# Performance work log

Measured on AMD Instinct MI355X. Metric: run time of the kernel, lower is better.

The kernel has to match this reference:

```python
import jax, jax.numpy as jnp
import numpy as np

B, N, D = 256, 50, 128
NEG = -9e15  # torch uses -9000000000000000.0
LEAKY_SLOPE = 0.2


def setup_inputs() -> dict:
    key = jax.random.key(0)
    ks = jax.random.split(key, 6)
    hidden = jax.random.normal(ks[0], (B, N, D), dtype=jnp.float32)
    adj = jax.random.randint(ks[1], (B, N, N), 0, 5)  # edge types 0..4
    a_0 = jax.random.normal(ks[2], (D, 1), dtype=jnp.float32) * 0.05
    a_1 = jax.random.normal(ks[3], (D, 1), dtype=jnp.float32) * 0.05
    a_2 = jax.random.normal(ks[4], (D, 1), dtype=jnp.float32) * 0.05
    a_3 = jax.random.normal(ks[5], (D, 1), dtype=jnp.float32) * 0.05
    return {"hidden": hidden, "adj": adj, "a_0": a_0, "a_1": a_1, "a_2": a_2, "a_3": a_3}


def reference(hidden, adj, a_0, a_1, a_2, a_3):
    # LocalAggregator.forward (typed-edge GAT over session graph).
    # Original builds a_input[b,i,j,:] = h[b,i,:]*h[b,j,:] (B,N,N,D) then
    # projects with 4 relation vectors a_k (D,1). We fuse: stack the 4
    # vectors and contract D in one einsum -> e[b,k,i,j].
    A = jnp.concatenate([a_0, a_1, a_2, a_3], axis=1)          # (D, 4)
    e = jnp.einsum('bid,bjd,dk->bkij', hidden, hidden, A)      # (B, 4, N, N)
    e = jax.nn.leaky_relu(e, negative_slope=LEAKY_SLOPE)
    # Per-edge-type masking: adj value v in {1..4} selects branch v-1,
    # anything else gets -9e15 (same chained torch.where semantics/order).
    scores = jnp.full_like(e[:, 0], NEG)                        # (B, N, N)
    scores = jnp.where(adj == 1, e[:, 0], scores)
    scores = jnp.where(adj == 2, e[:, 1], scores)
    scores = jnp.where(adj == 3, e[:, 2], scores)
    scores = jnp.where(adj == 4, e[:, 3], scores)
    attn = jax.nn.softmax(scores, axis=-1)                      # (B, N, N)
    return jnp.einsum('bij,bjd->bid', attn, hidden)             # (B, N, D)
```

## Files before the change

### kernel.cpp

```cpp
#include <hip/hip_runtime.h>
#include <stdint.h>

typedef __attribute__((ext_vector_type(8))) short short8;
typedef __attribute__((ext_vector_type(4))) float f32x4;

namespace {
constexpr int   kN     = 50;
constexpr int   kD     = 128;
constexpr float kNeg   = -9.0e15f;
constexpr float kSlope = 0.2f;
constexpr int   HS32   = 132;
constexpr int   HS16   = 136;
constexpr int   SS     = 68;
constexpr int   AS     = 52;
}

union Pack8 { uint32_t u[4]; short8 s; };

__global__ __launch_bounds__(512)
void gat_mfma_kernel(const float* __restrict__ hidden,
                     const int*   __restrict__ adj,
                     const float* __restrict__ a0,
                     const float* __restrict__ a1,
                     const float* __restrict__ a2,
                     const float* __restrict__ a3,
                     float* __restrict__ out)
{
    __shared__ float          Hf [kN * HS32];
    __shared__ unsigned short Hhi[kN * HS16];
    __shared__ unsigned short Hlo[kN * HS16];
    __shared__ float          Af [4 * HS32];
    __shared__ float          Sa [kN * SS];
    __shared__ float          Sb [kN * SS];
    __shared__ float          At [64 * AS];

    const int b    = blockIdx.x;
    const int tid  = threadIdx.x;
    const int lane = tid & 63;
    const int wid  = tid >> 6;

    const float* __restrict__ hb   = hidden + (size_t)b * (kN * kD);
    const int*   __restrict__ adjb = adj    + (size_t)b * (kN * kN);
    float*       __restrict__ outb = out    + (size_t)b * (kN * kD);

    const float4* hg = reinterpret_cast<const float4*>(hb);
    for (int idx = tid; idx < kN * (kD / 4); idx += 512) {
        const int j  = idx >> 5;
        const int d4 = idx & 31;
        const float4 v = hg[idx];
        *reinterpret_cast<float4*>(&Hf[j * HS32 + 4 * d4]) = v;

        const uint32_t u0 = __float_as_uint(v.x), u1 = __float_as_uint(v.y);
        const uint32_t u2 = __float_as_uint(v.z), u3 = __float_as_uint(v.w);
        const uint32_t h0 = u0 & 0xffff0000u, h1 = u1 & 0xffff0000u;
        const uint32_t h2 = u2 & 0xffff0000u, h3 = u3 & 0xffff0000u;
        uint2 hiw;
        hiw.x = h1 | (h0 >> 16);
        hiw.y = h3 | (h2 >> 16);
        const float r0 = v.x - __uint_as_float(h0);
        const float r1 = v.y - __uint_as_float(h1);
        const float r2 = v.z - __uint_as_float(h2);
        const float r3 = v.w - __uint_as_float(h3);
        uint2 low;
        low.x = (__float_as_uint(r1) & 0xffff0000u) | (__float_as_uint(r0) >> 16);
        low.y = (__float_as_uint(r3) & 0xffff0000u) | (__float_as_uint(r2) >> 16);
        *reinterpret_cast<uint2*>(&Hhi[j * HS16 + 4 * d4]) = hiw;
        *reinterpret_cast<uint2*>(&Hlo[j * HS16 + 4 * d4]) = low;
    }
    if (tid < 128) {
        const int k  = tid >> 5;
        const int d4 = tid & 31;
        const float* ap = (k == 0) ? a0 : (k == 1) ? a1 : (k == 2) ? a2 : a3;
        *reinterpret_cast<float4*>(&Af[k * HS32 + 4 * d4]) =
            *reinterpret_cast<const float4*>(ap + 4 * d4);
    }
    __syncthreads();

    {
        const int it = wid & 3;
        const int kh = wid >> 2;
        const int i0 = it * 16;
        const int g  = lane >> 4;
        const int f  = lane & 15;
        const int irow = (i0 + f < kN) ? (i0 + f) : (kN - 1);

        f32x4 acc[4][4];
        #pragma unroll
        for (int jt = 0; jt < 4; ++jt)
            #pragma unroll
            for (int k = 0; k < 4; ++k)
                acc[jt][k] = (f32x4){0.f, 0.f, 0.f, 0.f};

        #pragma unroll
        for (int ksl = 0; ksl < 2; ++ksl) {
            const int ks   = 2 * kh + ksl;
            const int dofs = 32 * ks + 8 * g;

            const float4 hA0 = *reinterpret_cast<const float4*>(&Hf[irow * HS32 + dofs]);
            const float4 hA1 = *reinterpret_cast<const float4*>(&Hf[irow * HS32 + dofs + 4]);
            float ha[8] = {hA0.x, hA0.y, hA0.z, hA0.w, hA1.x, hA1.y, hA1.z, hA1.w};

            short8 qhi[4], qlo[4];
            #pragma unroll
            for (int k = 0; k < 4; ++k) {
                const float4 av0 = *reinterpret_cast<const float4*>(&Af[k * HS32 + dofs]);
                const float4 av1 = *reinterpret_cast<const float4*>(&Af[k * HS32 + dofs + 4]);
                const float aa[8] = {av0.x, av0.y, av0.z, av0.w, av1.x, av1.y, av1.z, av1.w};
                Pack8 ph, pl;
                #pragma unroll
                for (int p = 0; p < 4; ++p) {
                    const float q0 = ha[2 * p]     * aa[2 * p];
                    const float q1 = ha[2 * p + 1] * aa[2 * p + 1];
                    const uint32_t b0 = __float_as_uint(q0) & 0xffff0000u;
                    const uint32_t b1 = __float_as_uint(q1) & 0xffff0000u;
                    ph.u[p] = b1 | (b0 >> 16);
                    const float s0 = q0 - __uint_as_float(b0);
                    const float s1 = q1 - __uint_as_float(b1);
                    pl.u[p] = (__float_as_uint(s1) & 0xffff0000u) | (__float_as_uint(s0) >> 16);
                }
                qhi[k] = ph.s;
                qlo[k] = pl.s;
            }

            #pragma unroll
            for (int jt = 0; jt < 4; ++jt) {
                const int jrow = (jt * 16 + f < kN) ? (jt * 16 + f) : (kN - 1);
                const short8 bh = *reinterpret_cast<const short8*>(&Hhi[jrow * HS16 + dofs]);
                const short8 bl = *reinterpret_cast<const short8*>(&Hlo[jrow * HS16 + dofs]);
                #pragma unroll
                for (int k = 0; k < 4; ++k) {
                    acc[jt][k] = __builtin_amdgcn_mfma_f32_16x16x32_bf16(qhi[k], bh, acc[jt][k], 0, 0, 0);
                    acc[jt][k] = __builtin_amdgcn_mfma_f32_16x16x32_bf16(qhi[k], bl, acc[jt][k], 0, 0, 0);
                    acc[jt][k] = __builtin_amdgcn_mfma_f32_16x16x32_bf16(qlo[k], bh, acc[jt][k], 0, 0, 0);
                }
            }
        }

        float* Sbuf = (kh == 0) ? Sa : Sb;
        #pragma unroll
        for (int jt = 0; jt < 4; ++jt) {
            const int j = jt * 16 + f;
            #pragma unroll
            for (int reg = 0; reg < 4; ++reg) {
                const int ii = i0 + 4 * g + reg;
                int adjv = 0;
                if (ii < kN && j < kN) adjv = adjb[ii * kN + j];
                const float val = (adjv == 1) ? acc[jt][0][reg]
                                : (adjv == 2) ? acc[jt][1][reg]
                                : (adjv == 3) ? acc[jt][2][reg]
                                : (adjv == 4) ? acc[jt][3][reg] : 0.f;
                if (ii < kN) Sbuf[ii * SS + j] = val;
            }
        }
    }
    __syncthreads();

    for (int r = wid; r < kN; r += 8) {
        const float x = Sa[r * SS + lane] + Sb[r * SS + lane];
        int adjv = 0;
        if (lane < kN) adjv = adjb[r * kN + lane];
        const bool valid = (adjv >= 1) && (adjv <= 4);
        const float lx = (x > 0.f) ? x : kSlope * x;
        float s = valid ? lx : kNeg;
        float m = s;
        #pragma unroll
        for (int o = 32; o; o >>= 1) m = fmaxf(m, __shfl_xor(m, o));
        const float e = (lane < kN) ? __expf(s - m) : 0.f;
        float t = e;
        #pragma unroll
        for (int o = 32; o; o >>= 1) t += __shfl_xor(t, o);
        At[lane * AS + r] = e / t;
    }
    __syncthreads();

    {
        const int it = wid & 3;
        const int dh = wid >> 2;
        const int i0 = it * 16;
        const int g  = lane >> 4;
        const int f  = lane & 15;
        const int db = 64 * dh + 4 * f;

        float4 o0 = {0.f, 0.f, 0.f, 0.f}, o1 = o0, o2 = o0, o3 = o0;
        #pragma unroll 5
        for (int j = 0; j < kN; ++j) {
            const float4 hv = *reinterpret_cast<const float4*>(&Hf[j * HS32 + db]);
            const float4 av = *reinterpret_cast<const float4*>(&At[j * AS + i0 + 4 * g]);
            o0.x += av.x * hv.x; o0.y += av.x * hv.y; o0.z += av.x * hv.z; o0.w += av.x * hv.w;
            o1.x += av.y * hv.x; o1.y += av.y * hv.y; o1.z += av.y * hv.z; o1.w += av.y * hv.w;
            o2.x += av.z * hv.x; o2.y += av.z * hv.y; o2.z += av.z * hv.z; o2.w += av.z * hv.w;
            o3.x += av.w * hv.x; o3.y += av.w * hv.y; o3.z += av.w * hv.z; o3.w += av.w * hv.w;
        }
        const int rbase = i0 + 4 * g;
        if (rbase + 0 < kN) *reinterpret_cast<float4*>(&outb[(rbase + 0) * kD + db]) = o0;
        if (rbase + 1 < kN) *reinterpret_cast<float4*>(&outb[(rbase + 1) * kD + db]) = o1;
        if (rbase + 2 < kN) *reinterpret_cast<float4*>(&outb[(rbase + 2) * kD + db]) = o2;
        if (rbase + 3 < kN) *reinterpret_cast<float4*>(&outb[(rbase + 3) * kD + db]) = o3;
    }
}

extern "C" void kernel_launch(void* const* d_in, const int* in_sizes, int n_in,
                              void* d_out, int out_size, void* d_ws, size_t ws_size,
                              hipStream_t stream) {
    const float* hidden = reinterpret_cast<const float*>(d_in[0]);
    const int*   adjp   = reinterpret_cast<const int*>(d_in[1]);
    const float* a0     = reinterpret_cast<const float*>(d_in[2]);
    const float* a1     = reinterpret_cast<const float*>(d_in[3]);
    const float* a2     = reinterpret_cast<const float*>(d_in[4]);
    const float* a3     = reinterpret_cast<const float*>(d_in[5]);
    float*       outp   = reinterpret_cast<float*>(d_out);

    gat_mfma_kernel<<<dim3(256), dim3(512), 0, stream>>>(
        hidden, adjp, a0, a1, a2, a3, outp);
}
```

Baseline: 20.06 us.

## Split each batch across two blocks by row halves and store attention as bf16

Launches two blocks per batch element, each handling half of the query rows, so 512 blocks run instead of 256. Each wave now owns one j-tile over the full D range, which removes the split-K partial score buffers and their reduction. The a_k vectors are read straight from global memory instead of staged in shared memory. Attention weights are stored as bf16 to cut LDS footprint. The trade-off is that hidden is loaded and split twice per batch, half the waves idle in the final aggregation, and bf16 attention weights lose precision.

```diff
diff --git a/kernel.cpp b/kernel.cpp
--- a/kernel.cpp
+++ b/kernel.cpp
@@ -12,48 +12,51 @@
 constexpr int   HS32   = 132;
 constexpr int   HS16   = 136;
 constexpr int   SS     = 68;
-constexpr int   AS     = 52;
+constexpr int   AS     = 36;
 }
 
 union Pack8 { uint32_t u[4]; short8 s; };
 
 __global__ __launch_bounds__(512)
-void gat_mfma_kernel(const float* __restrict__ hidden,
-                     const int*   __restrict__ adj,
-                     const float* __restrict__ a0,
-                     const float* __restrict__ a1,
-                     const float* __restrict__ a2,
-                     const float* __restrict__ a3,
-                     float* __restrict__ out)
+void gat_v6_kernel(const float* __restrict__ hidden,
+                   const int*   __restrict__ adj,
+                   const float* __restrict__ a0,
+                   const float* __restrict__ a1,
+                   const float* __restrict__ a2,
+                   const float* __restrict__ a3,
+                   float* __restrict__ out)
 {
     __shared__ float          Hf [kN * HS32];
-    __shared__ unsigned short Hhi[kN * HS16];
-    __shared__ unsigned short Hlo[kN * HS16];
-    __shared__ float          Af [4 * HS32];
-    __shared__ float          Sa [kN * SS];
-    __shared__ float          Sb [kN * SS];
-    __shared__ float          At [64 * AS];
-
-    const int b    = blockIdx.x;
+    __shared__ unsigned short Hhi[64 * HS16];
+    __shared__ unsigned short Hlo[64 * HS16];
+    __shared__ float          Sa [32 * SS];
+    __shared__ unsigned short At [64 * AS];
+
+    const int b    = blockIdx.x >> 1;
+    const int ih   = blockIdx.x & 1;
     const int tid  = threadIdx.x;
     const int lane = tid & 63;
-    const int wid  = tid >> 6;
+    const int wid  = __builtin_amdgcn_readfirstlane(tid >> 6);
+    const int g    = lane >> 4;
+    const int f    = lane & 15;
 
     const float* __restrict__ hb   = hidden + (size_t)b * (kN * kD);
     const int*   __restrict__ adjb = adj    + (size_t)b * (kN * kN);
     float*       __restrict__ outb = out    + (size_t)b * (kN * kD);
 
     const float4* hg = reinterpret_cast<const float4*>(hb);
-    for (int idx = tid; idx < kN * (kD / 4); idx += 512) {
-        const int j  = idx >> 5;
-        const int d4 = idx & 31;
-        const float4 v = hg[idx];
-        *reinterpret_cast<float4*>(&Hf[j * HS32 + 4 * d4]) = v;
-
-        const uint32_t u0 = __float_as_uint(v.x), u1 = __float_as_uint(v.y);
-        const uint32_t u2 = __float_as_uint(v.z), u3 = __float_as_uint(v.w);
-        const uint32_t h0 = u0 & 0xffff0000u, h1 = u1 & 0xffff0000u;
-        const uint32_t h2 = u2 & 0xffff0000u, h3 = u3 & 0xffff0000u;
+    #pragma unroll
+    for (int it4 = 0; it4 < 4; ++it4) {
+        const int idx = tid + it4 * 512;
+        const int j   = idx >> 5;
+        const int d4  = idx & 31;
+        float4 v = make_float4(0.f, 0.f, 0.f, 0.f);
+        if (j < kN) v = hg[j * 32 + d4];
+
+        const uint32_t h0 = __float_as_uint(v.x) & 0xffff0000u;
+        const uint32_t h1 = __float_as_uint(v.y) & 0xffff0000u;
+        const uint32_t h2 = __float_as_uint(v.z) & 0xffff0000u;
+        const uint32_t h3 = __float_as_uint(v.w) & 0xffff0000u;
         uint2 hiw;
         hiw.x = h1 | (h0 >> 16);
         hiw.y = h3 | (h2 >> 16);
@@ -66,45 +69,45 @@
         low.y = (__float_as_uint(r3) & 0xffff0000u) | (__float_as_uint(r2) >> 16);
         *reinterpret_cast<uint2*>(&Hhi[j * HS16 + 4 * d4]) = hiw;
         *reinterpret_cast<uint2*>(&Hlo[j * HS16 + 4 * d4]) = low;
-    }
-    if (tid < 128) {
-        const int k  = tid >> 5;
-        const int d4 = tid & 31;
-        const float* ap = (k == 0) ? a0 : (k == 1) ? a1 : (k == 2) ? a2 : a3;
-        *reinterpret_cast<float4*>(&Af[k * HS32 + 4 * d4]) =
-            *reinterpret_cast<const float4*>(ap + 4 * d4);
+        if (j < kN) *reinterpret_cast<float4*>(&Hf[j * HS32 + 4 * d4]) = v;
     }
     __syncthreads();
 
     {
-        const int it = wid & 3;
-        const int kh = wid >> 2;
-        const int i0 = it * 16;
-        const int g  = lane >> 4;
-        const int f  = lane & 15;
+        const int jt   = wid & 3;
+        const int itL  = wid >> 2;
+        const int itG  = 2 * ih + itL;
+        const int i0   = 16 * itG;
         const int irow = (i0 + f < kN) ? (i0 + f) : (kN - 1);
-
-        f32x4 acc[4][4];
-        #pragma unroll
-        for (int jt = 0; jt < 4; ++jt)
-            #pragma unroll
-            for (int k = 0; k < 4; ++k)
-                acc[jt][k] = (f32x4){0.f, 0.f, 0.f, 0.f};
-
-        #pragma unroll
-        for (int ksl = 0; ksl < 2; ++ksl) {
-            const int ks   = 2 * kh + ksl;
-            const int dofs = 32 * ks + 8 * g;
-
-            const float4 hA0 = *reinterpret_cast<const float4*>(&Hf[irow * HS32 + dofs]);
-            const float4 hA1 = *reinterpret_cast<const float4*>(&Hf[irow * HS32 + dofs + 4]);
-            float ha[8] = {hA0.x, hA0.y, hA0.z, hA0.w, hA1.x, hA1.y, hA1.z, hA1.w};
-
-            short8 qhi[4], qlo[4];
+        const int jrow = 16 * jt + f;
+
+        f32x4 acc[4];
+        #pragma unroll
+        for (int k = 0; k < 4; ++k) acc[k] = (f32x4){0.f, 0.f, 0.f, 0.f};
+
+        const float* __restrict__ aks[4] = {a0, a1, a2, a3};
+
+        #pragma unroll
+        for (int ksl = 0; ksl < 4; ++ksl) {
+            const int dofs = 32 * ksl + 8 * g;
+
+            const short8 ah8 = *reinterpret_cast<const short8*>(&Hhi[irow * HS16 + dofs]);
+            const short8 al8 = *reinterpret_cast<const short8*>(&Hlo[irow * HS16 + dofs]);
+            float ha[8];
+            #pragma unroll
+            for (int p = 0; p < 8; ++p) {
+                const uint32_t uh = ((uint32_t)(unsigned short)ah8[p]) << 16;
+                const uint32_t ul = ((uint32_t)(unsigned short)al8[p]) << 16;
+                ha[p] = __uint_as_float(uh) + __uint_as_float(ul);
+            }
+
+            const short8 bh = *reinterpret_cast<const short8*>(&Hhi[jrow * HS16 + dofs]);
+            const short8 bl = *reinterpret_cast<const short8*>(&Hlo[jrow * HS16 + dofs]);
+
             #pragma unroll
             for (int k = 0; k < 4; ++k) {
-                const float4 av0 = *reinterpret_cast<const float4*>(&Af[k * HS32 + dofs]);
-                const float4 av1 = *reinterpret_cast<const float4*>(&Af[k * HS32 + dofs + 4]);
+                const float4 av0 = *reinterpret_cast<const float4*>(aks[k] + dofs);
+                const float4 av1 = *reinterpret_cast<const float4*>(aks[k] + dofs + 4);
                 const float aa[8] = {av0.x, av0.y, av0.z, av0.w, av1.x, av1.y, av1.z, av1.w};
                 Pack8 ph, pl;
                 #pragma unroll
@@ -118,84 +121,89 @@
                     const float s1 = q1 - __uint_as_float(b1);
                     pl.u[p] = (__float_as_uint(s1) & 0xffff0000u) | (__float_as_uint(s0) >> 16);
                 }
-                qhi[k] = ph.s;
-                qlo[k] = pl.s;
-            }
-
-            #pragma unroll
-            for (int jt = 0; jt < 4; ++jt) {
-                const int jrow = (jt * 16 + f < kN) ? (jt * 16 + f) : (kN - 1);
-                const short8 bh = *reinterpret_cast<const short8*>(&Hhi[jrow * HS16 + dofs]);
-                const short8 bl = *reinterpret_cast<const short8*>(&Hlo[jrow * HS16 + dofs]);
-                #pragma unroll
-                for (int k = 0; k < 4; ++k) {
-                    acc[jt][k] = __builtin_amdgcn_mfma_f32_16x16x32_bf16(qhi[k], bh, acc[jt][k], 0, 0, 0);
-                    acc[jt][k] = __builtin_amdgcn_mfma_f32_16x16x32_bf16(qhi[k], bl, acc[jt][k], 0, 0, 0);
-                    acc[jt][k] = __builtin_amdgcn_mfma_f32_16x16x32_bf16(qlo[k], bh, acc[jt][k], 0, 0, 0);
-                }
-            }
-        }
-
-        float* Sbuf = (kh == 0) ? Sa : Sb;
-        #pragma unroll
-        for (int jt = 0; jt < 4; ++jt) {
-            const int j = jt * 16 + f;
-            #pragma unroll
-            for (int reg = 0; reg < 4; ++reg) {
-                const int ii = i0 + 4 * g + reg;
-                int adjv = 0;
-                if (ii < kN && j < kN) adjv = adjb[ii * kN + j];
-                const float val = (adjv == 1) ? acc[jt][0][reg]
-                                : (adjv == 2) ? acc[jt][1][reg]
-                                : (adjv == 3) ? acc[jt][2][reg]
-                                : (adjv == 4) ? acc[jt][3][reg] : 0.f;
-                if (ii < kN) Sbuf[ii * SS + j] = val;
+                acc[k] = __builtin_amdgcn_mfma_f32_16x16x32_bf16(ph.s, bh, acc[k], 0, 0, 0);
+                acc[k] = __builtin_amdgcn_mfma_f32_16x16x32_bf16(ph.s, bl, acc[k], 0, 0, 0);
+                acc[k] = __builtin_amdgcn_mfma_f32_16x16x32_bf16(pl.s, bh, acc[k], 0, 0, 0);
+            }
+        }
+
+        const int j = 16 * jt + f;
+        #pragma unroll
+        for (int reg = 0; reg < 4; ++reg) {
+            const int iL = 16 * itL + 4 * g + reg;
+            const int ii = 32 * ih + iL;
+            if (ii < kN && j < kN) {
+                const int adjv = adjb[ii * kN + j];
+                const float val = (adjv == 1) ? acc[0][reg]
+                                : (adjv == 2) ? acc[1][reg]
+                                : (adjv == 3) ? acc[2][reg]
+                                : (adjv == 4) ? acc[3][reg] : 0.f;
+                Sa[iL * SS + j] = val;
             }
         }
     }
     __syncthreads();
 
-    for (int r = wid; r < kN; r += 8) {
-        const float x = Sa[r * SS + lane] + Sb[r * SS + lane];
-        int adjv = 0;
-        if (lane < kN) adjv = adjb[r * kN + lane];
-        const bool valid = (adjv >= 1) && (adjv <= 4);
-        const float lx = (x > 0.f) ? x : kSlope * x;
-        float s = valid ? lx : kNeg;
-        float m = s;
-        #pragma unroll
-        for (int o = 32; o; o >>= 1) m = fmaxf(m, __shfl_xor(m, o));
-        const float e = (lane < kN) ? __expf(s - m) : 0.f;
-        float t = e;
-        #pragma unroll
-        for (int o = 32; o; o >>= 1) t += __shfl_xor(t, o);
-        At[lane * AS + r] = e / t;
+    {
+        const int icount = ih ? (kN - 32) : 32;
+        float attv[4];
+        #pragma unroll
+        for (int t = 0; t < 4; ++t) {
+            const int rL = wid + 8 * t;
+            const int r  = 32 * ih + rL;
+            const bool rowv = (rL < icount);
+            const float x = Sa[rL * SS + lane];
+            int adjv = 0;
+            if (rowv && lane < kN) adjv = adjb[r * kN + lane];
+            const bool valid = (adjv >= 1) && (adjv <= 4);
+            const float lx = (x > 0.f) ? x : kSlope * x;
+            float s = valid ? lx : kNeg;
+            float m = s;
+            #pragma unroll
+            for (int o = 32; o; o >>= 1) m = fmaxf(m, __shfl_xor(m, o));
+            const float e = (lane < kN) ? __expf(s - m) : 0.f;
+            float ts = e;
+            #pragma unroll
+            for (int o = 32; o; o >>= 1) ts += __shfl_xor(ts, o);
+            attv[t] = e / ts;
+        }
+        #pragma unroll
+        for (int t = 0; t < 4; ++t) {
+            const int rL = wid + 8 * t;
+            if (rL < icount) {
+                uint32_t u = __float_as_uint(attv[t]);
+                u += 0x7fffu + ((u >> 16) & 1u);
+                At[lane * AS + rL] = (unsigned short)(u >> 16);
+            }
+        }
     }
     __syncthreads();
 
-    {
-        const int it = wid & 3;
-        const int dh = wid >> 2;
-        const int i0 = it * 16;
-        const int g  = lane >> 4;
-        const int f  = lane & 15;
-        const int db = 64 * dh + 4 * f;
-
-        float4 o0 = {0.f, 0.f, 0.f, 0.f}, o1 = o0, o2 = o0, o3 = o0;
+    if (wid < 4) {
+        const int itL = wid & 1;
+        const int dh  = wid >> 1;
+        const int i0L = 16 * itL;
+        const int db  = 64 * dh + 4 * f;
+
+        f32x4 o0 = {0.f, 0.f, 0.f, 0.f}, o1 = o0, o2 = o0, o3 = o0;
         #pragma unroll 5
         for (int j = 0; j < kN; ++j) {
-            const float4 hv = *reinterpret_cast<const float4*>(&Hf[j * HS32 + db]);
-            const float4 av = *reinterpret_cast<const float4*>(&At[j * AS + i0 + 4 * g]);
-            o0.x += av.x * hv.x; o0.y += av.x * hv.y; o0.z += av.x * hv.z; o0.w += av.x * hv.w;
-            o1.x += av.y * hv.x; o1.y += av.y * hv.y; o1.z += av.y * hv.z; o1.w += av.y * hv.w;
-            o2.x += av.z * hv.x; o2.y += av.z * hv.y; o2.z += av.z * hv.z; o2.w += av.z * hv.w;
-            o3.x += av.w * hv.x; o3.y += av.w * hv.y; o3.z += av.w * hv.z; o3.w += av.w * hv.w;
-        }
-        const int rbase = i0 + 4 * g;
-        if (rbase + 0 < kN) *reinterpret_cast<float4*>(&outb[(rbase + 0) * kD + db]) = o0;
-        if (rbase + 1 < kN) *reinterpret_cast<float4*>(&outb[(rbase + 1) * kD + db]) = o1;
-        if (rbase + 2 < kN) *reinterpret_cast<float4*>(&outb[(rbase + 2) * kD + db]) = o2;
-        if (rbase + 3 < kN) *reinterpret_cast<float4*>(&outb[(rbase + 3) * kD + db]) = o3;
+            const float4  hv = *reinterpret_cast<const float4*>(&Hf[j * HS32 + db]);
+            const ushort4 a4 = *reinterpret_cast<const ushort4*>(&At[j * AS + i0L + 4 * g]);
+            const float av0 = __uint_as_float(((uint32_t)a4.x) << 16);
+            const float av1 = __uint_as_float(((uint32_t)a4.y) << 16);
+            const float av2 = __uint_as_float(((uint32_t)a4.z) << 16);
+            const float av3 = __uint_as_float(((uint32_t)a4.w) << 16);
+            o0.x += av0 * hv.x; o0.y += av0 * hv.y; o0.z += av0 * hv.z; o0.w += av0 * hv.w;
+            o1.x += av1 * hv.x; o1.y += av1 * hv.y; o1.z += av1 * hv.z; o1.w += av1 * hv.w;
+            o2.x += av2 * hv.x; o2.y += av2 * hv.y; o2.z += av2 * hv.z; o2.w += av2 * hv.w;
+            o3.x += av3 * hv.x; o3.y += av3 * hv.y; o3.z += av3 * hv.z; o3.w += av3 * hv.w;
+        }
+        const int iiB = 32 * ih + i0L + 4 * g;
+        if (iiB + 0 < kN) *reinterpret_cast<f32x4*>(&outb[(iiB + 0) * kD + db]) = o0;
+        if (iiB + 1 < kN) *reinterpret_cast<f32x4*>(&outb[(iiB + 1) * kD + db]) = o1;
+        if (iiB + 2 < kN) *reinterpret_cast<f32x4*>(&outb[(iiB + 2) * kD + db]) = o2;
+        if (iiB + 3 < kN) *reinterpret_cast<f32x4*>(&outb[(iiB + 3) * kD + db]) = o3;
     }
 }
 
@@ -210,6 +218,6 @@
     const float* a3     = reinterpret_cast<const float*>(d_in[5]);
     float*       outp   = reinterpret_cast<float*>(d_out);
 
-    gat_mfma_kernel<<<dim3(256), dim3(512), 0, stream>>>(
+    gat_v6_kernel<<<dim3(512), dim3(512), 0, stream>>>(
         hidden, adjp, a0, a1, a2, a3, outp);
 }
```

Result: slower. 20.65 us (+3.0%).
